# Kernel optimization log

Hardware: AMD Instinct MI355X
Metric: run time of the kernel (lower is better)

Reference implementation:

```python
import jax, jax.numpy as jnp
import numpy as np

N_E = 8192
E_DIM = 64
BETA = 0.25
N_TOKENS = 32768


def setup_inputs() -> dict:
    key = jax.random.key(0)
    k1, k2 = jax.random.split(key)
    x = jax.random.normal(k1, (N_TOKENS, E_DIM), dtype=jnp.float32)
    # nn.Embedding weight initialized uniform(-1/n_e, 1/n_e)
    codebook = jax.random.uniform(k2, (N_E, E_DIM), dtype=jnp.float32,
                                  minval=-1.0 / N_E, maxval=1.0 / N_E)
    return {"x": x, "codebook": codebook, "start": 0, "end": N_E, "use_sk": 0}


def reference(x, codebook, start, end, use_sk):
    # use_sk=0 -> argmin branch (sinkhorn branch calls external helper, not exercised)
    latent = x.reshape(-1, E_DIM)                       # [N, D]
    cb = codebook[start:end]                            # [K, D]
    # squared euclidean distances: ||z||^2 + ||e||^2 - 2 z.e
    d = (jnp.sum(latent * latent, axis=1, keepdims=True)
         + jnp.sum(cb * cb, axis=1)[None, :]
         - 2.0 * jnp.einsum('nd,kd->nk', latent, cb))   # [N, K]
    indices = jnp.argmin(d, axis=-1) + start            # [N]
    x_q = codebook[indices].reshape(x.shape)            # gather
    sg = jax.lax.stop_gradient
    commitment_loss = jnp.mean((sg(x_q) - x) ** 2)
    codebook_loss = jnp.mean((x_q - sg(x)) ** 2)
    loss = codebook_loss + BETA * commitment_loss
    x_q_st = x + sg(x_q - x)                            # straight-through estimator
    indices = indices.reshape(x.shape[:-1])
    return x_q_st, loss, indices
```

## Files before the change

### kernel.cpp

```cpp
#include <hip/hip_runtime.h>
#include <math.h>


#define N_E    8192
#define EDIM   64
#define NTOK   32768
#define NELEM  (NTOK * EDIM)
#define CSZ    32
#define WINDOW 3e-4f
#define TTOK   256
#define TCODE  2048
#define SROW   72
#define TOKB   16
#define CCAP   64
#define KCAP   288

typedef __attribute__((ext_vector_type(8)))  short          short8;
typedef __attribute__((ext_vector_type(8)))  unsigned short ushort8v;
typedef __attribute__((ext_vector_type(16))) float          f32x16;

__device__ __forceinline__ unsigned short f2bf(float f) {
  unsigned int u = __float_as_uint(f);
  return (unsigned short)((u + 0x7FFFu + ((u >> 16) & 1u)) >> 16);
}
__device__ __forceinline__ unsigned short f2h(float f) {
  union { _Float16 h; unsigned short u; } cv; cv.h = (_Float16)f; return cv.u;
}
__device__ __forceinline__ float h2f(unsigned short b) {
  union { _Float16 h; unsigned short u; } cv; cv.u = b; return (float)cv.h;
}
__device__ __forceinline__ float max16(const f32x16 a) {
  float m0 = fmaxf(fmaxf(a[0], a[1]),   fmaxf(a[2], a[3]));
  float m1 = fmaxf(fmaxf(a[4], a[5]),   fmaxf(a[6], a[7]));
  float m2 = fmaxf(fmaxf(a[8], a[9]),   fmaxf(a[10], a[11]));
  float m3 = fmaxf(fmaxf(a[12], a[13]), fmaxf(a[14], a[15]));
  return fmaxf(fmaxf(m0, m1), fmaxf(m2, m3));
}
__device__ __forceinline__ float sx_of(const float4* xl4) {
#pragma clang fp contract(off)
  float a0=0,a1=0,a2=0,a3=0,a4=0,a5=0,a6=0,a7=0;
#pragma unroll
  for (int i = 0; i < 8; ++i) {
    float4 pA = xl4[2*i], pB = xl4[2*i+1];
    a0 += pA.x * pA.x; a1 += pA.y * pA.y; a2 += pA.z * pA.z; a3 += pA.w * pA.w;
    a4 += pB.x * pB.x; a5 += pB.y * pB.y; a6 += pB.z * pB.z; a7 += pB.w * pB.w;
  }
  return ((a0+a1) + (a2+a3)) + ((a4+a5) + (a6+a7));
}

__global__ __launch_bounds__(256) void vq_sc(const float* __restrict__ cb,
                                             float* __restrict__ sc,
                                             unsigned short* __restrict__ cbf) {
#pragma clang fp contract(off)
  int r = blockIdx.x * 256 + threadIdx.x;
  const float4* c4 = (const float4*)(cb + (size_t)r * EDIM);
  float sval = sx_of(c4);
  sc[r] = sval;
  unsigned short* dst = cbf + (size_t)r * EDIM;
#pragma unroll
  for (int h = 0; h < 8; ++h) {
    float4 fA = c4[2*h], fB = c4[2*h+1];
    ushort8v o = {f2bf(fA.x), f2bf(fA.y), f2bf(fA.z), f2bf(fA.w),
                  f2bf(fB.x), f2bf(fB.y), f2bf(fB.z), f2bf(fB.w)};
    *(ushort8v*)&dst[h * 8] = o;
  }
}

__global__ __launch_bounds__(256, 2) void vq_pass1(
    const float* __restrict__ x, const unsigned short* __restrict__ cbf,
    unsigned int* __restrict__ cand,
    const int* __restrict__ p_start, const int* __restrict__ p_end) {
  __shared__ unsigned short Cs[128 * SROW];
  int tid = threadIdx.x;
  int tb = blockIdx.x;
  int cbk = blockIdx.y;
  int s = *p_start, e = *p_end;

  int lane = tid & 63, wv = tid >> 6;
  int half = lane >> 5, ln = lane & 31;
  int tokbase = wv * 64;

  const ushort8v* cg0 = (const ushort8v*)(cbf + (size_t)cbk * TCODE * EDIM);
#pragma unroll
  for (int p = 0; p < 4; ++p) {
    int idx = tid + p * 256;
    int row = idx >> 3, h = idx & 7;
    *(ushort8v*)&Cs[row * SROW + h * 8] = cg0[idx];
  }

  short8 bfr[2][4];
#pragma unroll
  for (int tg = 0; tg < 2; ++tg) {
    const float* xrow =
        x + (size_t)(tb * TTOK + tokbase + tg * 32 + ln) * EDIM + half * 8;
#pragma unroll
    for (int ks = 0; ks < 4; ++ks) {
      float4 fA = *(const float4*)(xrow + ks * 16);
      float4 fB = *(const float4*)(xrow + ks * 16 + 4);
      short8 v = {(short)f2bf(fA.x), (short)f2bf(fA.y), (short)f2bf(fA.z),
                  (short)f2bf(fA.w), (short)f2bf(fB.x), (short)f2bf(fB.y),
                  (short)f2bf(fB.z), (short)f2bf(fB.w)};
      bfr[tg][ks] = v;
    }
  }
  __syncthreads();

  unsigned s0=~0u,s1=~0u,s2=~0u,s3=~0u,s4=~0u,s5=~0u,s6=~0u,s7=~0u,s8=~0u;
  unsigned m0=0,m1=0,m2=0,m3=0,m4=0,m5=0,m6=0,m7=0,m8=0;
  unsigned long long bmap = 0ull;
  float lminf = INFINITY;

  for (int nb = 0; nb < 16; ++nb) {
    ushort8v creg[4];
    if (nb < 15) {
      const ushort8v* cg =
          (const ushort8v*)(cbf + ((size_t)cbk * TCODE + (nb + 1) * 128) * EDIM);
#pragma unroll
      for (int p = 0; p < 4; ++p) creg[p] = cg[tid + p * 256];
    }
    f32x16 acc[2][4];
#pragma unroll
    for (int tg = 0; tg < 2; ++tg)
#pragma unroll
      for (int ct = 0; ct < 4; ++ct) acc[tg][ct] = (f32x16)0.0f;
#pragma unroll
    for (int ks = 0; ks < 4; ++ks)
#pragma unroll
      for (int ct = 0; ct < 4; ++ct) {
        short8 a = *(const short8*)&Cs[(ct*32 + ln) * SROW + ks*16 + half*8];
        acc[0][ct] = __builtin_amdgcn_mfma_f32_32x32x16_bf16(a, bfr[0][ks],
                                                             acc[0][ct], 0, 0, 0);
        acc[1][ct] = __builtin_amdgcn_mfma_f32_32x32x16_bf16(a, bfr[1][ks],
                                                             acc[1][ct], 0, 0, 0);
      }
    __syncthreads();
    if (nb < 15) {
#pragma unroll
      for (int p = 0; p < 4; ++p) {
        int idx = tid + p * 256;
        int row = idx >> 3, h = idx & 7;
        *(ushort8v*)&Cs[row * SROW + h * 8] = creg[p];
      }
    }
    int cbase0 = cbk * TCODE + nb * 128;
#pragma unroll
    for (int ct = 0; ct < 4; ++ct) {
      int c0 = cbase0 + ct * 32;
      bool full = (c0 >= s) && (c0 + 32 <= e);
      float v0, v1;
      if (full) {
        v0 = max16(acc[0][ct]);
        v1 = max16(acc[1][ct]);
      } else {
        v0 = -INFINITY; v1 = -INFINITY;
#pragma unroll
        for (int r = 0; r < 16; ++r) {
          int code = c0 + (r & 3) + 8 * (r >> 2) + 4 * half;
          if (code >= s && code < e) {
            v0 = fmaxf(v0, acc[0][ct][r]);
            v1 = fmaxf(v1, acc[1][ct][r]);
          }
        }
      }
      v0 = fmaxf(v0, __shfl_xor(v0, 32, 64));
      v1 = fmaxf(v1, __shfl_xor(v1, 32, 64));
      float t0 = v0 - WINDOW * 0.5f;
      float t1 = v1 - WINDOW * 0.5f;
      unsigned b0 = 0, b1 = 0;
#pragma unroll
      for (int r = 0; r < 16; ++r) {
        int pos = (r & 3) + 8 * (r >> 2) + 4 * half;
        if (acc[0][ct][r] >= t0) b0 |= (1u << pos);
        if (acc[1][ct][r] >= t1) b1 |= (1u << pos);
      }
      b0 |= __shfl_xor(b0, 32, 64);
      b1 |= __shfl_xor(b1, 32, 64);
      float vs = half ? v1 : v0;
      unsigned bs = half ? b1 : b0;
      unsigned short hh = f2h(-2.0f * vs);
      float mvf = h2f(hh);
      lminf = fminf(lminf, mvf);
      if (mvf <= lminf + WINDOW) {
        bmap |= 1ull << (nb * 4 + ct);
        unsigned mono = (unsigned)hh ^ ((hh & 0x8000u) ? 0xFFFFu : 0x8000u);
        unsigned p = (mono << 16) | (unsigned)(nb * 4 + ct);
        unsigned pm = bs;
        if (p < s8) {
#define INS2_(SK, SM) { bool lt_ = p < (SK); unsigned tk_ = (SK), tm_ = (SM); \
          if (lt_) { (SK) = p; (SM) = pm; p = tk_; pm = tm_; } }
          INS2_(s0,m0) INS2_(s1,m1) INS2_(s2,m2) INS2_(s3,m3) INS2_(s4,m4)
          INS2_(s5,m5) INS2_(s6,m6) INS2_(s7,m7) INS2_(s8,m8)
#undef INS2_
        }
      }
    }
    __syncthreads();
  }

  {
    float thr = lminf + WINDOW;
    unsigned rec[8], msk[8];
#define EMIT_(J, S, M) { unsigned mono_ = (S) >> 16; \
    unsigned hh_ = (mono_ & 0x8000u) ? (mono_ ^ 0x8000u) : (mono_ ^ 0xFFFFu); \
    float v_ = h2f((unsigned short)hh_); \
    rec[J] = (v_ <= thr) ? ((hh_ << 16) | ((S) & 0xFFFFu)) : 0xFFFFFFFFu; \
    msk[J] = (M); }
    EMIT_(0, s0, m0) EMIT_(1, s1, m1) EMIT_(2, s2, m2) EMIT_(3, s3, m3)
    EMIT_(4, s4, m4) EMIT_(5, s5, m5) EMIT_(6, s6, m6) EMIT_(7, s7, m7)
#undef EMIT_
    {
      unsigned mono_ = s8 >> 16;
      unsigned hh_ = (mono_ & 0x8000u) ? (mono_ ^ 0x8000u) : (mono_ ^ 0xFFFFu);
      float v8 = h2f((unsigned short)hh_);
      if (v8 <= thr) rec[7] = 0x0000FFFEu;
    }
    int token = tb * TTOK + tokbase + lane;
#pragma unroll
    for (int j = 0; j < 8; ++j) {
      cand[(size_t)(cbk * 8 + j) * NTOK + token] = rec[j];
      cand[(size_t)(32 + cbk * 8 + j) * NTOK + token] = msk[j];
    }
    cand[(size_t)(64 + cbk * 2) * NTOK + token] = (unsigned)(bmap & 0xFFFFFFFFull);
    cand[(size_t)(65 + cbk * 2) * NTOK + token] = (unsigned)(bmap >> 32);
  }
}

__global__ __launch_bounds__(256) void vq_rescue(
    const float* __restrict__ x, const float* __restrict__ cb,
    const float* __restrict__ sc, const unsigned int* __restrict__ cand,
    float* __restrict__ out_xq, float* __restrict__ out_idx,
    float* __restrict__ partial,
    const int* __restrict__ p_start, const int* __restrict__ p_end) {
#pragma clang fp contract(off)
  __shared__ float xsh[TOKB][64];
  __shared__ float sxs[TOKB];
  __shared__ unsigned short lst[TOKB][CCAP];
  __shared__ unsigned short clst[TOKB][KCAP];
  __shared__ int ccnt[TOKB], kcnt[TOKB];
  int tid  = threadIdx.x;
  int wv   = tid >> 6;
  int lane = tid & 63;
  int blk  = blockIdx.x;
  int s = *p_start, e = *p_end;

  if (tid < TOKB) { ccnt[tid] = 0; kcnt[tid] = 0; }
#pragma unroll
  for (int p = 0; p < (TOKB * CCAP) / 256; ++p)
    ((unsigned short*)lst)[tid + p * 256] = 0xFFFFu;
  __syncthreads();

  if (tid < 64) {
    int tl = tid >> 2, q = tid & 3;
    int gtok = blk * TOKB + tl;
    unsigned rv[8], mk[8];
#pragma unroll
    for (int j = 0; j < 8; ++j) {
      rv[j] = cand[(size_t)(q * 8 + j) * NTOK + gtok];
      mk[j] = cand[(size_t)(32 + q * 8 + j) * NTOK + gtok];
    }
    float m = INFINITY;
#pragma unroll
    for (int j = 0; j < 8; ++j) {
      unsigned cid = rv[j] & 0xFFFFu;
      float v = (cid < 64u) ? h2f((unsigned short)(rv[j] >> 16)) : INFINITY;
      m = fminf(m, v);
    }
    m = fminf(m, __shfl_xor(m, 1, 64));
    m = fminf(m, __shfl_xor(m, 2, 64));
    float thr = m + WINDOW;
    bool marker = ((rv[7] & 0xFFFFu) == 0xFFFEu);
    if (!marker) {
#pragma unroll
      for (int j = 0; j < 8; ++j) {
        unsigned cid = rv[j] & 0xFFFFu;
        if (cid < 64u && h2f((unsigned short)(rv[j] >> 16)) <= thr) {
          unsigned bits = mk[j];
          int n = __popc(bits);
          int base = atomicAdd(&ccnt[tl], n);
          if (base + n <= CCAP) {
            int kb = (q * 64 + (int)cid) * CSZ;
            while (bits) {
              int bpos = __ffs(bits) - 1; bits &= bits - 1;
              lst[tl][base++] = (unsigned short)(kb + bpos);
            }
          } else {
            int kb2 = atomicAdd(&kcnt[tl], 1);
            if (kb2 < KCAP) clst[tl][kb2] = (unsigned short)(q * 64 + (int)cid);
          }
        }
      }
    } else {
      unsigned cid0 = rv[0] & 0xFFFFu;
      float v0 = (cid0 < 64u) ? h2f((unsigned short)(rv[0] >> 16)) : INFINITY;
      if (v0 <= thr) {
        unsigned b0 = cand[(size_t)(64 + q * 2) * NTOK + gtok];
        unsigned b1 = cand[(size_t)(65 + q * 2) * NTOK + gtok];
        int n = __popc(b0) + __popc(b1);
        int base = atomicAdd(&kcnt[tl], n);
        while (b0) { int j = __ffs(b0) - 1; b0 &= b0 - 1;
          if (base < KCAP) clst[tl][base] = (unsigned short)(q * 64 + j); ++base; }
        while (b1) { int j = __ffs(b1) - 1; b1 &= b1 - 1;
          if (base < KCAP) clst[tl][base] = (unsigned short)(q * 64 + 32 + j); ++base; }
      }
    }
  } else if (tid < 192) {
    int t = tid - 64;
    int tl = t >> 3, seg = t & 7;
    const float4* xg = (const float4*)(x + (size_t)(blk * TOKB + tl) * EDIM + seg * 8);
    float4 A = xg[0], B = xg[1];
    *(float4*)&xsh[tl][seg * 8]     = A;
    *(float4*)&xsh[tl][seg * 8 + 4] = B;
  } else if (tid < 192 + TOKB) {
    int tl = tid - 192;
    sxs[tl] = sx_of((const float4*)(x + (size_t)(blk * TOKB + tl) * EDIM));
  }
  __syncthreads();

#define EVAL_CODE_BODY(K_, XL4) do {                                           \
    const float4* c4_ = (const float4*)(cb + (size_t)(K_) * EDIM);             \
    float t0_=0.0f,t1_=0.0f,t2_=0.0f,t3_=0.0f;                                 \
    _Pragma("unroll")                                                          \
    for (int i_ = 0; i_ < 8; ++i_) {                 \
      float4 v_ = c4_[2*i_ + h5_];                                             \
      float4 p_ = (XL4)[2*i_ + h5_];                                           \
      t0_ += v_.x * p_.x; t1_ += v_.y * p_.y;                                  \
      t2_ += v_.z * p_.z; t3_ += v_.w * p_.w;                                  \
    }                                                                          \
    s2_ = (t0_ + t1_) + (t2_ + t3_);              \
  } while (0)

#define FINISH_CODE(K_, ACT, SX, BP) do {                                      \
    float tt_ = s2_ + __shfl_xor(s2_, 1, 64);                                  \
    if ((ACT) && (K_) >= s && (K_) < e) {                                      \
      float d_ = ((SX) + sc[K_]) - 2.0f * tt_;                                 \
      unsigned db_ = __float_as_uint(d_);                                      \
      unsigned en_ = db_ ^ ((unsigned)((int)db_ >> 31) | 0x80000000u);         \
      unsigned long long pk_ = ((unsigned long long)en_ << 32) | (unsigned)(K_);\
      if (pk_ < (BP)) (BP) = pk_;                                              \
    }                                                                          \
  } while (0)

  float sg[4];
#pragma unroll
  for (int ti = 0; ti < 4; ++ti) {
    int tl = wv * 4 + ti;
    int gtok = blk * TOKB + tl;
    const float4* xl4 = (const float4*)xsh[tl];
    float sx = sxs[tl];
    unsigned long long bp = ~0ull;
    int ci_ = lane >> 1, h5_ = lane & 1;
    int nc = ccnt[tl]; if (nc > CCAP) nc = CCAP;
    for (int b0 = 0; b0 < nc; b0 += 32) {
      int nb = nc - b0; if (nb > 32) nb = 32;
      int kraw = (ci_ < nb) ? (int)lst[tl][b0 + ci_] : 0xFFFF;
      bool act = (kraw != 0xFFFF);
      int k_ = act ? kraw : 0;
      float s2_ = 0.0f;
      if (act) EVAL_CODE_BODY(k_, xl4);
      FINISH_CODE(k_, act, sx, bp);
    }
    int nk = kcnt[tl]; if (nk > KCAP) nk = KCAP;
    for (int i = 0; i < nk; ++i) {
      int k_ = (int)clst[tl][i] * CSZ + ci_;
      float s2_;
      EVAL_CODE_BODY(k_, xl4);
      FINISH_CODE(k_, true, sx, bp);
    }
#pragma unroll
    for (int off = 32; off >= 1; off >>= 1) {
      unsigned long long o = __shfl_xor(bp, off, 64);
      if (o < bp) bp = o;
    }
    int bidx = (int)(unsigned)(bp & 0xFFFFFFFFull) & (N_E - 1);

    float xx = xsh[tl][lane];
    float qv = cb[(size_t)bidx * EDIM + lane];
    float diff = qv - xx;
    out_xq[(size_t)gtok * EDIM + lane] = xx + diff;
    if (lane == 0) out_idx[gtok] = (float)bidx;
    float l = diff * diff;
#pragma unroll
    for (int off = 32; off >= 1; off >>= 1) l += __shfl_down(l, off, 64);
    sg[ti] = l;
  }
#undef EVAL_CODE_BODY
#undef FINISH_CODE
  if (lane == 0)
    partial[blk * 4 + wv] = (sg[0] + sg[1]) + (sg[2] + sg[3]);
}

__global__ __launch_bounds__(256) void vq_loss(const float* __restrict__ partial,
                                               float* __restrict__ out_loss) {
  int tid = threadIdx.x;
  float s = 0.0f;
  for (int i = tid; i < NTOK / 4; i += 256) s += partial[i];
#pragma unroll
  for (int off = 32; off >= 1; off >>= 1) s += __shfl_down(s, off, 64);
  __shared__ float sdata[4];
  if ((tid & 63) == 0) sdata[tid >> 6] = s;
  __syncthreads();
  if (tid == 0) {
    float total = (sdata[0] + sdata[1]) + (sdata[2] + sdata[3]);
    float m = total * (1.0f / (float)NELEM);
    out_loss[0] = m + 0.25f * m;
  }
}

extern "C" void kernel_launch(void* const* d_in, const int* in_sizes, int n_in,
                              void* d_out, int out_size, void* d_ws, size_t ws_size,
                              hipStream_t stream) {
  const float* x  = (const float*)d_in[0];
  const float* cb = (const float*)d_in[1];
  const int* p_start = (const int*)d_in[2];
  const int* p_end   = (const int*)d_in[3];

  float* ws = (float*)d_ws;
  float* sc      = ws;
  float* partial = ws + N_E;
  unsigned short* cbf  = (unsigned short*)(ws + 2 * N_E);
  unsigned int*   cand = (unsigned int*)(cbf + (size_t)N_E * EDIM);

  float* out      = (float*)d_out;
  float* out_xq   = out;
  float* out_loss = out + NELEM;
  float* out_idx  = out + NELEM + 1;

  vq_sc<<<N_E / 256, 256, 0, stream>>>(cb, sc, cbf);
  dim3 g1(NTOK / TTOK, N_E / TCODE);
  vq_pass1<<<g1, 256, 0, stream>>>(x, cbf, cand, p_start, p_end);
  vq_rescue<<<NTOK / TOKB, 256, 0, stream>>>(x, cb, sc, cand, out_xq, out_idx,
                                             partial, p_start, p_end);
  vq_loss<<<1, 256, 0, stream>>>(partial, out_loss);
}
```

Baseline: 183.1 us.

## Halve pass1 codebook chunk, split accumulators, raise occupancy to three blocks

Pass 1 now gives each block 1024 codes instead of 2048, so the grid gets twice as many blocks along the codebook axis (8 chunks instead of 4). Each 128-code tile is processed as two halves of two accumulator tiles, which lowers register pressure, and launch bounds now request three blocks per CU. The per-half running minimum is tracked for both token groups so the bitmask pass can be skipped when neither tile is in the window. The candidate buffer layout and the pass2 merge change to match: eight chunks, 32-bit bitmaps, 128 merging threads and a larger KCAP. The cost is twice the candidate records written and read, and more merge work per token.

After: 179.0 us. 2.2% less time.

```diff
diff --git a/kernel.cpp b/kernel.cpp
--- a/kernel.cpp
+++ b/kernel.cpp
@@ -9,11 +9,11 @@
 #define CSZ    32
 #define WINDOW 3e-4f
 #define TTOK   256
-#define TCODE  2048
+#define TCODE  1024
 #define SROW   72
 #define TOKB   16
 #define CCAP   64
-#define KCAP   288
+#define KCAP   320
 
 typedef __attribute__((ext_vector_type(8)))  short          short8;
 typedef __attribute__((ext_vector_type(8)))  unsigned short ushort8v;
@@ -30,11 +30,14 @@
   union { _Float16 h; unsigned short u; } cv; cv.u = b; return (float)cv.h;
 }
 __device__ __forceinline__ float max16(const f32x16 a) {
-  float m0 = fmaxf(fmaxf(a[0], a[1]),   fmaxf(a[2], a[3]));
-  float m1 = fmaxf(fmaxf(a[4], a[5]),   fmaxf(a[6], a[7]));
-  float m2 = fmaxf(fmaxf(a[8], a[9]),   fmaxf(a[10], a[11]));
-  float m3 = fmaxf(fmaxf(a[12], a[13]), fmaxf(a[14], a[15]));
-  return fmaxf(fmaxf(m0, m1), fmaxf(m2, m3));
+  float m = fmaxf(fmaxf(a[0], a[1]), a[2]);
+  m = fmaxf(fmaxf(m, a[3]),  a[4]);
+  m = fmaxf(fmaxf(m, a[5]),  a[6]);
+  m = fmaxf(fmaxf(m, a[7]),  a[8]);
+  m = fmaxf(fmaxf(m, a[9]),  a[10]);
+  m = fmaxf(fmaxf(m, a[11]), a[12]);
+  m = fmaxf(fmaxf(m, a[13]), a[14]);
+  return fmaxf(m, a[15]);
 }
 __device__ __forceinline__ float sx_of(const float4* xl4) {
 #pragma clang fp contract(off)
@@ -66,7 +69,7 @@
   }
 }
 
-__global__ __launch_bounds__(256, 2) void vq_pass1(
+__global__ __launch_bounds__(256, 3) void vq_pass1(
     const float* __restrict__ x, const unsigned short* __restrict__ cbf,
     unsigned int* __restrict__ cand,
     const int* __restrict__ p_start, const int* __restrict__ p_end) {
@@ -107,34 +110,97 @@
 
   unsigned s0=~0u,s1=~0u,s2=~0u,s3=~0u,s4=~0u,s5=~0u,s6=~0u,s7=~0u,s8=~0u;
   unsigned m0=0,m1=0,m2=0,m3=0,m4=0,m5=0,m6=0,m7=0,m8=0;
-  unsigned long long bmap = 0ull;
-  float lminf = INFINITY;
-
-  for (int nb = 0; nb < 16; ++nb) {
+  unsigned bmap = 0u;
+  float lm0 = INFINITY, lm1 = INFINITY;
+
+  for (int nb = 0; nb < 8; ++nb) {
     ushort8v creg[4];
-    if (nb < 15) {
+    if (nb < 7) {
       const ushort8v* cg =
           (const ushort8v*)(cbf + ((size_t)cbk * TCODE + (nb + 1) * 128) * EDIM);
 #pragma unroll
       for (int p = 0; p < 4; ++p) creg[p] = cg[tid + p * 256];
     }
-    f32x16 acc[2][4];
-#pragma unroll
-    for (int tg = 0; tg < 2; ++tg)
-#pragma unroll
-      for (int ct = 0; ct < 4; ++ct) acc[tg][ct] = (f32x16)0.0f;
-#pragma unroll
-    for (int ks = 0; ks < 4; ++ks)
-#pragma unroll
-      for (int ct = 0; ct < 4; ++ct) {
-        short8 a = *(const short8*)&Cs[(ct*32 + ln) * SROW + ks*16 + half*8];
-        acc[0][ct] = __builtin_amdgcn_mfma_f32_32x32x16_bf16(a, bfr[0][ks],
-                                                             acc[0][ct], 0, 0, 0);
-        acc[1][ct] = __builtin_amdgcn_mfma_f32_32x32x16_bf16(a, bfr[1][ks],
-                                                             acc[1][ct], 0, 0, 0);
+#pragma unroll
+    for (int cp = 0; cp < 2; ++cp) {
+      f32x16 acc[2][2];
+#pragma unroll
+      for (int tg = 0; tg < 2; ++tg)
+#pragma unroll
+        for (int c2 = 0; c2 < 2; ++c2) acc[tg][c2] = (f32x16)0.0f;
+#pragma unroll
+      for (int ks = 0; ks < 4; ++ks)
+#pragma unroll
+        for (int c2 = 0; c2 < 2; ++c2) {
+          int ct = cp * 2 + c2;
+          short8 a = *(const short8*)&Cs[(ct*32 + ln) * SROW + ks*16 + half*8];
+          acc[0][c2] = __builtin_amdgcn_mfma_f32_32x32x16_bf16(a, bfr[0][ks],
+                                                               acc[0][c2], 0, 0, 0);
+          acc[1][c2] = __builtin_amdgcn_mfma_f32_32x32x16_bf16(a, bfr[1][ks],
+                                                               acc[1][c2], 0, 0, 0);
+        }
+#pragma unroll
+      for (int c2 = 0; c2 < 2; ++c2) {
+        int cidL = nb * 4 + cp * 2 + c2;
+        int c0 = cbk * TCODE + cidL * 32;
+        bool full = (c0 >= s) && (c0 + 32 <= e);
+        float v0, v1;
+        if (full) {
+          v0 = max16(acc[0][c2]);
+          v1 = max16(acc[1][c2]);
+        } else {
+          v0 = -INFINITY; v1 = -INFINITY;
+#pragma unroll
+          for (int r = 0; r < 16; ++r) {
+            int code = c0 + (r & 3) + 8 * (r >> 2) + 4 * half;
+            if (code >= s && code < e) {
+              v0 = fmaxf(v0, acc[0][c2][r]);
+              v1 = fmaxf(v1, acc[1][c2][r]);
+            }
+          }
+        }
+        v0 = fmaxf(v0, __shfl_xor(v0, 32, 64));
+        v1 = fmaxf(v1, __shfl_xor(v1, 32, 64));
+        unsigned short hh0 = f2h(-2.0f * v0);
+        unsigned short hh1 = f2h(-2.0f * v1);
+        float mv0 = h2f(hh0), mv1 = h2f(hh1);
+        lm0 = fminf(lm0, mv0);
+        lm1 = fminf(lm1, mv1);
+        bool a0 = (mv0 <= lm0 + WINDOW);
+        bool a1 = (mv1 <= lm1 + WINDOW);
+        unsigned b0 = 0, b1 = 0;
+        if (a0 | a1) {
+          float t0 = v0 - WINDOW * 0.5f;
+          float t1 = v1 - WINDOW * 0.5f;
+#pragma unroll
+          for (int r = 0; r < 16; ++r) {
+            int pos = (r & 3) + 8 * (r >> 2) + 4 * half;
+            if (acc[0][c2][r] >= t0) b0 |= (1u << pos);
+            if (acc[1][c2][r] >= t1) b1 |= (1u << pos);
+          }
+          b0 |= __shfl_xor(b0, 32, 64);
+          b1 |= __shfl_xor(b1, 32, 64);
+        }
+        bool aown = half ? a1 : a0;
+        if (aown) {
+          bmap |= 1u << cidL;
+          unsigned short hh = half ? hh1 : hh0;
+          unsigned bs = half ? b1 : b0;
+          unsigned mono = (unsigned)hh ^ ((hh & 0x8000u) ? 0xFFFFu : 0x8000u);
+          unsigned p = (mono << 16) | (unsigned)cidL;
+          unsigned pm = bs;
+          if (p < s8) {
+#define INS2_(SK, SM) { bool lt_ = p < (SK); unsigned tk_ = (SK), tm_ = (SM); \
+            if (lt_) { (SK) = p; (SM) = pm; p = tk_; pm = tm_; } }
+            INS2_(s0,m0) INS2_(s1,m1) INS2_(s2,m2) INS2_(s3,m3) INS2_(s4,m4)
+            INS2_(s5,m5) INS2_(s6,m6) INS2_(s7,m7) INS2_(s8,m8)
+#undef INS2_
+          }
+        }
       }
+    }
     __syncthreads();
-    if (nb < 15) {
+    if (nb < 7) {
 #pragma unroll
       for (int p = 0; p < 4; ++p) {
         int idx = tid + p * 256;
@@ -142,62 +208,11 @@
         *(ushort8v*)&Cs[row * SROW + h * 8] = creg[p];
       }
     }
-    int cbase0 = cbk * TCODE + nb * 128;
-#pragma unroll
-    for (int ct = 0; ct < 4; ++ct) {
-      int c0 = cbase0 + ct * 32;
-      bool full = (c0 >= s) && (c0 + 32 <= e);
-      float v0, v1;
-      if (full) {
-        v0 = max16(acc[0][ct]);
-        v1 = max16(acc[1][ct]);
-      } else {
-        v0 = -INFINITY; v1 = -INFINITY;
-#pragma unroll
-        for (int r = 0; r < 16; ++r) {
-          int code = c0 + (r & 3) + 8 * (r >> 2) + 4 * half;
-          if (code >= s && code < e) {
-            v0 = fmaxf(v0, acc[0][ct][r]);
-            v1 = fmaxf(v1, acc[1][ct][r]);
-          }
-        }
-      }
-      v0 = fmaxf(v0, __shfl_xor(v0, 32, 64));
-      v1 = fmaxf(v1, __shfl_xor(v1, 32, 64));
-      float t0 = v0 - WINDOW * 0.5f;
-      float t1 = v1 - WINDOW * 0.5f;
-      unsigned b0 = 0, b1 = 0;
-#pragma unroll
-      for (int r = 0; r < 16; ++r) {
-        int pos = (r & 3) + 8 * (r >> 2) + 4 * half;
-        if (acc[0][ct][r] >= t0) b0 |= (1u << pos);
-        if (acc[1][ct][r] >= t1) b1 |= (1u << pos);
-      }
-      b0 |= __shfl_xor(b0, 32, 64);
-      b1 |= __shfl_xor(b1, 32, 64);
-      float vs = half ? v1 : v0;
-      unsigned bs = half ? b1 : b0;
-      unsigned short hh = f2h(-2.0f * vs);
-      float mvf = h2f(hh);
-      lminf = fminf(lminf, mvf);
-      if (mvf <= lminf + WINDOW) {
-        bmap |= 1ull << (nb * 4 + ct);
-        unsigned mono = (unsigned)hh ^ ((hh & 0x8000u) ? 0xFFFFu : 0x8000u);
-        unsigned p = (mono << 16) | (unsigned)(nb * 4 + ct);
-        unsigned pm = bs;
-        if (p < s8) {
-#define INS2_(SK, SM) { bool lt_ = p < (SK); unsigned tk_ = (SK), tm_ = (SM); \
-          if (lt_) { (SK) = p; (SM) = pm; p = tk_; pm = tm_; } }
-          INS2_(s0,m0) INS2_(s1,m1) INS2_(s2,m2) INS2_(s3,m3) INS2_(s4,m4)
-          INS2_(s5,m5) INS2_(s6,m6) INS2_(s7,m7) INS2_(s8,m8)
-#undef INS2_
-        }
-      }
-    }
     __syncthreads();
   }
 
   {
+    float lminf = half ? lm1 : lm0;
     float thr = lminf + WINDOW;
     unsigned rec[8], msk[8];
 #define EMIT_(J, S, M) { unsigned mono_ = (S) >> 16; \
@@ -218,10 +233,9 @@
 #pragma unroll
     for (int j = 0; j < 8; ++j) {
       cand[(size_t)(cbk * 8 + j) * NTOK + token] = rec[j];
-      cand[(size_t)(32 + cbk * 8 + j) * NTOK + token] = msk[j];
-    }
-    cand[(size_t)(64 + cbk * 2) * NTOK + token] = (unsigned)(bmap & 0xFFFFFFFFull);
-    cand[(size_t)(65 + cbk * 2) * NTOK + token] = (unsigned)(bmap >> 32);
+      cand[(size_t)(64 + cbk * 8 + j) * NTOK + token] = msk[j];
+    }
+    cand[(size_t)(128 + cbk) * NTOK + token] = bmap;
   }
 }
 
@@ -249,67 +263,67 @@
     ((unsigned short*)lst)[tid + p * 256] = 0xFFFFu;
   __syncthreads();
 
-  if (tid < 64) {
-    int tl = tid >> 2, q = tid & 3;
+  if (tid < 128) {
+    int tl = tid >> 3, q = tid & 7;
     int gtok = blk * TOKB + tl;
     unsigned rv[8], mk[8];
 #pragma unroll
     for (int j = 0; j < 8; ++j) {
       rv[j] = cand[(size_t)(q * 8 + j) * NTOK + gtok];
-      mk[j] = cand[(size_t)(32 + q * 8 + j) * NTOK + gtok];
+      mk[j] = cand[(size_t)(64 + q * 8 + j) * NTOK + gtok];
     }
     float m = INFINITY;
 #pragma unroll
     for (int j = 0; j < 8; ++j) {
       unsigned cid = rv[j] & 0xFFFFu;
-      float v = (cid < 64u) ? h2f((unsigned short)(rv[j] >> 16)) : INFINITY;
+      float v = (cid < 32u) ? h2f((unsigned short)(rv[j] >> 16)) : INFINITY;
       m = fminf(m, v);
     }
     m = fminf(m, __shfl_xor(m, 1, 64));
     m = fminf(m, __shfl_xor(m, 2, 64));
+    m = fminf(m, __shfl_xor(m, 4, 64));
     float thr = m + WINDOW;
     bool marker = ((rv[7] & 0xFFFFu) == 0xFFFEu);
     if (!marker) {
 #pragma unroll
       for (int j = 0; j < 8; ++j) {
         unsigned cid = rv[j] & 0xFFFFu;
-        if (cid < 64u && h2f((unsigned short)(rv[j] >> 16)) <= thr) {
+        if (cid < 32u && h2f((unsigned short)(rv[j] >> 16)) <= thr) {
           unsigned bits = mk[j];
           int n = __popc(bits);
           int base = atomicAdd(&ccnt[tl], n);
           if (base + n <= CCAP) {
-            int kb = (q * 64 + (int)cid) * CSZ;
+            int kb = (q * 32 + (int)cid) * CSZ;
             while (bits) {
               int bpos = __ffs(bits) - 1; bits &= bits - 1;
               lst[tl][base++] = (unsigned short)(kb + bpos);
             }
           } else {
             int kb2 = atomicAdd(&kcnt[tl], 1);
-            if (kb2 < KCAP) clst[tl][kb2] = (unsigned short)(q * 64 + (int)cid);
+            if (kb2 < KCAP) clst[tl][kb2] = (unsigned short)(q * 32 + (int)cid);
           }
         }
       }
     } else {
       unsigned cid0 = rv[0] & 0xFFFFu;
-      float v0 = (cid0 < 64u) ? h2f((unsigned short)(rv[0] >> 16)) : INFINITY;
+      float v0 = (cid0 < 32u) ? h2f((unsigned short)(rv[0] >> 16)) : INFINITY;
       if (v0 <= thr) {
-        unsigned b0 = cand[(size_t)(64 + q * 2) * NTOK + gtok];
-        unsigned b1 = cand[(size_t)(65 + q * 2) * NTOK + gtok];
-        int n = __popc(b0) + __popc(b1);
+        unsigned b0 = cand[(size_t)(128 + q) * NTOK + gtok];
+        int n = __popc(b0);
         int base = atomicAdd(&kcnt[tl], n);
         while (b0) { int j = __ffs(b0) - 1; b0 &= b0 - 1;
-          if (base < KCAP) clst[tl][base] = (unsigned short)(q * 64 + j); ++base; }
-        while (b1) { int j = __ffs(b1) - 1; b1 &= b1 - 1;
-          if (base < KCAP) clst[tl][base] = (unsigned short)(q * 64 + 32 + j); ++base; }
+          if (base < KCAP) clst[tl][base] = (unsigned short)(q * 32 + j); ++base; }
       }
     }
   } else if (tid < 192) {
-    int t = tid - 64;
-    int tl = t >> 3, seg = t & 7;
-    const float4* xg = (const float4*)(x + (size_t)(blk * TOKB + tl) * EDIM + seg * 8);
-    float4 A = xg[0], B = xg[1];
-    *(float4*)&xsh[tl][seg * 8]     = A;
-    *(float4*)&xsh[tl][seg * 8 + 4] = B;
+    int t = tid - 128;
+#pragma unroll
+    for (int p = 0; p < 4; ++p) {
+      int idx = t + p * 64;
+      int tl = idx >> 4, seg = idx & 15;
+      *(float4*)&xsh[tl][seg * 4] =
+          ((const float4*)(x + (size_t)(blk * TOKB + tl) * EDIM))[seg];
+    }
   } else if (tid < 192 + TOKB) {
     int tl = tid - 192;
     sxs[tl] = sx_of((const float4*)(x + (size_t)(blk * TOKB + tl) * EDIM));
```
